# Performance work log

Measured on AMD Instinct MI355X. Metric: run time of the kernel, lower is better.

## Reference

```python
import jax, jax.numpy as jnp
import numpy as np

INPUT_SIZE = 64 * 64 * 10  # 40960
H1, H2, H3 = 256, 32, 32
BATCH = 2048


def _linear_init(key, out_f, in_f):
    # torch nn.Linear default init: U(-1/sqrt(in_f), 1/sqrt(in_f))
    kw, kb = jax.random.split(key)
    bound = 1.0 / np.sqrt(in_f)
    W = jax.random.uniform(kw, (out_f, in_f), jnp.float32, -bound, bound)
    b = jax.random.uniform(kb, (out_f,), jnp.float32, -bound, bound)
    return W, b


def setup_inputs() -> dict:
    key = jax.random.key(0)
    ks = jax.random.split(key, 7)
    input_player = jax.random.uniform(ks[0], (BATCH, INPUT_SIZE), jnp.float32)
    input_opponent = jax.random.uniform(ks[1], (BATCH, INPUT_SIZE), jnp.float32)
    W1p, b1p = _linear_init(ks[2], H1, INPUT_SIZE)
    W1o, b1o = _linear_init(ks[3], H1, INPUT_SIZE)
    W2, b2 = _linear_init(ks[4], H2, 2 * H1)
    W3, b3 = _linear_init(ks[5], H3, H2)
    Wo, bo = _linear_init(ks[6], 1, H3)
    return {
        "input_player": input_player, "input_opponent": input_opponent,
        "W1p": W1p, "b1p": b1p, "W1o": W1o, "b1o": b1o,
        "W2": W2, "b2": b2, "W3": W3, "b3": b3, "Wo": Wo, "bo": bo,
    }


def _crelu(x):
    # ReLU followed by clamp(0, 1) == clipped ReLU
    return jnp.clip(x, 0.0, 1.0)


def reference(input_player, input_opponent, W1p, b1p, W1o, b1o, W2, b2, W3, b3, Wo, bo):
    # Feature transformer (sparse-in-practice 40960 -> 256 per perspective)
    acc_p = _crelu(input_player @ W1p.T + b1p)    # [B, 256]
    acc_o = _crelu(input_opponent @ W1o.T + b1o)  # [B, 256]
    combined = jnp.concatenate([acc_p, acc_o], axis=-1)  # [B, 512]
    h = _crelu(combined @ W2.T + b2)  # [B, 32]
    h = _crelu(h @ W3.T + b3)         # [B, 32]
    out = _crelu(h @ Wo.T + bo)       # [B, 1]
    return out
```

## Files before the change

kernel.cpp:

```cpp
#include <hip/hip_runtime.h>

#define K_DIM 40960
#define NFEAT 256
#define BATCH 2048

typedef _Float16 f16;
typedef _Float16 f16x8 __attribute__((ext_vector_type(8)));
typedef _Float16 f16x4 __attribute__((ext_vector_type(4)));
typedef _Float16 f16x2 __attribute__((ext_vector_type(2)));
typedef float f32x4 __attribute__((ext_vector_type(4)));

__global__ __launch_bounds__(256) void convert_w(
    const float* __restrict__ w1p, const float* __restrict__ w1o,
    f16* __restrict__ w16p, f16* __restrict__ w16o) {
  const long N4 = (long)NFEAT * K_DIM / 4;
  long stride = (long)gridDim.x * blockDim.x;
  for (long i = (long)blockIdx.x * blockDim.x + threadIdx.x; i < 2 * N4; i += stride) {
    const float4* src;
    f16* dst;
    long idx;
    if (i < N4) { src = (const float4*)w1p; dst = w16p; idx = i; }
    else        { src = (const float4*)w1o; dst = w16o; idx = i - N4; }
    float4 v = src[idx];
    f16x4 h;
    h[0] = (f16)v.x; h[1] = (f16)v.y; h[2] = (f16)v.z; h[3] = (f16)v.w;
    *(f16x4*)(dst + idx * 4) = h;
  }
}

__global__ __launch_bounds__(512, 4) void ft_gemm(
    const float* __restrict__ Ap, const float* __restrict__ Ao,
    const f16* __restrict__ W16p, const f16* __restrict__ W16o,
    int S, f16* __restrict__ partials) {
  __shared__ f16 Ash[64 * 64];
  __shared__ f16 Wsh[256 * 64];

  const int b = blockIdx.x;
  const int G = 2 * S;
  const int g = b % G;
  const int mt = b / G;
  const int persp = g & 1;
  const int s = g >> 1;
  const int mbase = mt * 64;

  const float* A = persp ? Ao : Ap;
  const f16* W16 = persp ? W16o : W16p;

  const int tid = threadIdx.x;
  const int lane = tid & 63;
  const int wv = tid >> 6;
  const int mrow = lane & 15;
  const int kq = lane >> 4;

  f32x4 acc[4][2];
#pragma unroll
  for (int rt = 0; rt < 4; ++rt)
#pragma unroll
    for (int ct = 0; ct < 2; ++ct)
      acc[rt][ct] = (f32x4){0.f, 0.f, 0.f, 0.f};

  const int krange = K_DIM / S;
  const int kstart = s * krange;
  const int kend = kstart + krange;

  int a_row[2], a_cb[2];
#pragma unroll
  for (int i = 0; i < 2; ++i) { int f = i * 512 + tid; a_row[i] = f >> 4; a_cb[i] = f & 15; }
  int w_rl[4], w_kbs[4], w_kbg[4];
#pragma unroll
  for (int i = 0; i < 4; ++i) {
    int f = i * 512 + tid; w_rl[i] = f >> 3; w_kbs[i] = f & 7; w_kbg[i] = w_kbs[i] ^ (w_rl[i] & 7);
  }

  float4 pa[2];
  f16x8 pw[4];
#pragma unroll
  for (int i = 0; i < 2; ++i)
    pa[i] = *(const float4*)(A + (size_t)(mbase + a_row[i]) * K_DIM + kstart + a_cb[i] * 4);
#pragma unroll
  for (int i = 0; i < 4; ++i)
    pw[i] = *(const f16x8*)(W16 + (size_t)w_rl[i] * K_DIM + kstart + w_kbg[i] * 8);

  for (int k0 = kstart; k0 < kend; k0 += 64) {
#pragma unroll
    for (int i = 0; i < 2; ++i) {
      int row = a_row[i], cb = a_cb[i];
      int slot = (cb >> 1) ^ (row & 7);
      f16x4 h;
      h[0] = (f16)pa[i].x; h[1] = (f16)pa[i].y; h[2] = (f16)pa[i].z; h[3] = (f16)pa[i].w;
      *(f16x4*)&Ash[row * 64 + slot * 8 + (cb & 1) * 4] = h;
    }
#pragma unroll
    for (int i = 0; i < 4; ++i)
      *(f16x8*)&Wsh[w_rl[i] * 64 + w_kbs[i] * 8] = pw[i];
    __syncthreads();

    const int kn = (k0 + 64 < kend) ? (k0 + 64) : kstart;
#pragma unroll
    for (int i = 0; i < 2; ++i)
      pa[i] = *(const float4*)(A + (size_t)(mbase + a_row[i]) * K_DIM + kn + a_cb[i] * 4);
#pragma unroll
    for (int i = 0; i < 4; ++i)
      pw[i] = *(const f16x8*)(W16 + (size_t)w_rl[i] * K_DIM + kn + w_kbg[i] * 8);

#pragma unroll
    for (int ks = 0; ks < 2; ++ks) {
      const int kb = ks * 4 + kq;
      f16x8 af[4], bf[2];
#pragma unroll
      for (int rt = 0; rt < 4; ++rt) {
        int row = rt * 16 + mrow;
        af[rt] = *(const f16x8*)&Ash[row * 64 + (kb ^ (row & 7)) * 8];
      }
#pragma unroll
      for (int ct = 0; ct < 2; ++ct) {
        int rown = (wv * 2 + ct) * 16 + mrow;
        bf[ct] = *(const f16x8*)&Wsh[rown * 64 + (kb ^ (rown & 7)) * 8];
      }
#pragma unroll
      for (int rt = 0; rt < 4; ++rt)
#pragma unroll
        for (int ct = 0; ct < 2; ++ct)
          acc[rt][ct] = __builtin_amdgcn_mfma_f32_16x16x32_f16(af[rt], bf[ct], acc[rt][ct], 0, 0, 0);
    }
    __syncthreads();
  }

  f16* pp = partials + (size_t)g * ((size_t)BATCH * NFEAT);
#pragma unroll
  for (int rt = 0; rt < 4; ++rt)
#pragma unroll
    for (int ct = 0; ct < 2; ++ct) {
      int col = (wv * 2 + ct) * 16 + mrow;
#pragma unroll
      for (int i = 0; i < 4; ++i) {
        int row = mbase + rt * 16 + kq * 4 + i;
        pp[(size_t)row * NFEAT + col] = (f16)acc[rt][ct][i];
      }
    }
}

__global__ __launch_bounds__(256) void reduce_bias(
    const f16* __restrict__ partials, const float* __restrict__ b1p,
    const float* __restrict__ b1o, int S, float* __restrict__ combined) {
  int idx = blockIdx.x * 256 + threadIdx.x;
  int r = idx >> 8;
  int c2 = idx & 255;
  int persp = c2 >> 7;
  int n = (c2 & 127) * 2;
  const float* bias = persp ? b1o : b1p;
  float s0 = bias[n], s1 = bias[n + 1];
#pragma unroll 4
  for (int s = 0; s < S; ++s) {
    f16x2 v = *(const f16x2*)(partials + ((size_t)(s * 2 + persp)) * BATCH * NFEAT +
                              (size_t)r * NFEAT + n);
    s0 += (float)v[0]; s1 += (float)v[1];
  }
  s0 = fminf(fmaxf(s0, 0.f), 1.f);
  s1 = fminf(fmaxf(s1, 0.f), 1.f);
  float2 o; o.x = s0; o.y = s1;
  *(float2*)(combined + (size_t)r * 512 + persp * 256 + n) = o;
}

__global__ __launch_bounds__(256) void mlp(
    const float* __restrict__ combined, const float* __restrict__ W2,
    const float* __restrict__ b2, const float* __restrict__ W3,
    const float* __restrict__ b3, const float* __restrict__ Wo,
    const float* __restrict__ bo, float* __restrict__ out) {
  __shared__ f16 W2T[512 * 33];
  __shared__ float H1s[8][33];
  __shared__ float H2s[8][33];
  int tid = threadIdx.x;
#pragma unroll
  for (int i = 0; i < 64; ++i) {
    int idx = i * 256 + tid;
    int j = idx >> 9;
    int k = idx & 511;
    W2T[k * 33 + j] = (f16)W2[idx];
  }
  __syncthreads();

  int lr = tid >> 5;
  int j = tid & 31;
  int r = blockIdx.x * 8 + lr;

  const float* crow = combined + (size_t)r * 512;
  float acc = b2[j];
#pragma unroll 8
  for (int k = 0; k < 512; ++k) acc += crow[k] * (float)W2T[k * 33 + j];
  H1s[lr][j] = fminf(fmaxf(acc, 0.f), 1.f);
  __syncthreads();

  acc = b3[j];
  const float* w3r = W3 + j * 32;
#pragma unroll
  for (int k = 0; k < 32; ++k) acc += H1s[lr][k] * w3r[k];
  H2s[lr][j] = fminf(fmaxf(acc, 0.f), 1.f);
  __syncthreads();

  if (j == 0) {
    float o = bo[0];
#pragma unroll
    for (int k = 0; k < 32; ++k) o += H2s[lr][k] * Wo[k];
    out[r] = fminf(fmaxf(o, 0.f), 1.f);
  }
}

extern "C" void kernel_launch(void* const* d_in, const int* in_sizes, int n_in,
                              void* d_out, int out_size, void* d_ws, size_t ws_size,
                              hipStream_t stream) {
  const float* Ap  = (const float*)d_in[0];
  const float* Ao  = (const float*)d_in[1];
  const float* W1p = (const float*)d_in[2];
  const float* b1p = (const float*)d_in[3];
  const float* W1o = (const float*)d_in[4];
  const float* b1o = (const float*)d_in[5];
  const float* W2  = (const float*)d_in[6];
  const float* b2  = (const float*)d_in[7];
  const float* W3  = (const float*)d_in[8];
  const float* b3  = (const float*)d_in[9];
  const float* Wo  = (const float*)d_in[10];
  const float* bo  = (const float*)d_in[11];
  float* out = (float*)d_out;

  const size_t W16B = 2UL * NFEAT * K_DIM * 2;
  const size_t COMB = (size_t)BATCH * 512 * 4;
  auto need = [&](int s) {
    return W16B + (size_t)s * 2 * BATCH * NFEAT * 2 + COMB;
  };

  int S = 16;
  while (S > 1 && need(S) > ws_size) S >>= 1;

  char* ws = (char*)d_ws;
  f16* W16p = (f16*)ws;
  f16* W16o = W16p + (size_t)NFEAT * K_DIM;
  f16* partials = (f16*)(ws + W16B);
  float* combined = (float*)(ws + W16B + (size_t)S * 2 * BATCH * NFEAT * 2);

  convert_w<<<1024, 256, 0, stream>>>(W1p, W1o, W16p, W16o);

  int grid = (BATCH / 64) * S * 2;
  ft_gemm<<<grid, 512, 0, stream>>>(Ap, Ao, W16p, W16o, S, partials);

  reduce_bias<<<(BATCH * 256) / 256, 256, 0, stream>>>(partials, b1p, b1o, S, combined);

  mlp<<<BATCH / 8, 256, 0, stream>>>(combined, W2, b2, W3, b3, Wo, bo, out);
}
```

Before: 779.8 us.

## Keep W fragments in registers, double-buffer A tile, switch to 32x32 MFMA

The feature-transformer GEMM no longer stages the W tile through shared memory. Each wave now loads its 32-column W fragments straight from global memory into registers, with two register sets prefetched alternately. The A tile is double-buffered in LDS, so each iteration needs one barrier instead of two, and the MFMA shape changes from 16x16x32 to 32x32x16. The split-K factor drops from 16 to 8, which cuts partial-sum traffic and reduce work but leaves fewer blocks. This trades LDS traffic and barriers for higher register pressure and uncoalesced-per-row global W loads.

```diff
diff --git a/kernel.cpp b/kernel.cpp
--- a/kernel.cpp
+++ b/kernel.cpp
@@ -9,6 +9,7 @@
 typedef _Float16 f16x4 __attribute__((ext_vector_type(4)));
 typedef _Float16 f16x2 __attribute__((ext_vector_type(2)));
 typedef float f32x4 __attribute__((ext_vector_type(4)));
+typedef float f32x16 __attribute__((ext_vector_type(16)));
 
 __global__ __launch_bounds__(256) void convert_w(
     const float* __restrict__ w1p, const float* __restrict__ w1o,
@@ -32,8 +33,7 @@
     const float* __restrict__ Ap, const float* __restrict__ Ao,
     const f16* __restrict__ W16p, const f16* __restrict__ W16o,
     int S, f16* __restrict__ partials) {
-  __shared__ f16 Ash[64 * 64];
-  __shared__ f16 Wsh[256 * 64];
+  __shared__ f16 Ash[2][64 * 64];
 
   const int b = blockIdx.x;
   const int G = 2 * S;
@@ -49,94 +49,115 @@
   const int tid = threadIdx.x;
   const int lane = tid & 63;
   const int wv = tid >> 6;
-  const int mrow = lane & 15;
-  const int kq = lane >> 4;
-
-  f32x4 acc[4][2];
-#pragma unroll
-  for (int rt = 0; rt < 4; ++rt)
-#pragma unroll
-    for (int ct = 0; ct < 2; ++ct)
-      acc[rt][ct] = (f32x4){0.f, 0.f, 0.f, 0.f};
+  const int l31 = lane & 31;
+  const int hi = lane >> 5;
 
   const int krange = K_DIM / S;
   const int kstart = s * krange;
-  const int kend = kstart + krange;
-
-  int a_row[2], a_cb[2];
-#pragma unroll
-  for (int i = 0; i < 2; ++i) { int f = i * 512 + tid; a_row[i] = f >> 4; a_cb[i] = f & 15; }
-  int w_rl[4], w_kbs[4], w_kbg[4];
-#pragma unroll
-  for (int i = 0; i < 4; ++i) {
-    int f = i * 512 + tid; w_rl[i] = f >> 3; w_kbs[i] = f & 7; w_kbg[i] = w_kbs[i] ^ (w_rl[i] & 7);
-  }
-
-  float4 pa[2];
-  f16x8 pw[4];
-#pragma unroll
-  for (int i = 0; i < 2; ++i)
-    pa[i] = *(const float4*)(A + (size_t)(mbase + a_row[i]) * K_DIM + kstart + a_cb[i] * 4);
-#pragma unroll
-  for (int i = 0; i < 4; ++i)
-    pw[i] = *(const f16x8*)(W16 + (size_t)w_rl[i] * K_DIM + kstart + w_kbg[i] * 8);
-
-  for (int k0 = kstart; k0 < kend; k0 += 64) {
-#pragma unroll
-    for (int i = 0; i < 2; ++i) {
-      int row = a_row[i], cb = a_cb[i];
-      int slot = (cb >> 1) ^ (row & 7);
-      f16x4 h;
-      h[0] = (f16)pa[i].x; h[1] = (f16)pa[i].y; h[2] = (f16)pa[i].z; h[3] = (f16)pa[i].w;
-      *(f16x4*)&Ash[row * 64 + slot * 8 + (cb & 1) * 4] = h;
+  const int nit = krange / 64;
+
+  const int f0 = tid, f1 = tid + 512;
+  const int ar0 = f0 >> 4, ac0 = f0 & 15;
+  const int ar1 = f1 >> 4, ac1 = f1 & 15;
+  const float* pA0 = A + (size_t)(mbase + ar0) * K_DIM + ac0 * 4;
+  const float* pA1 = A + (size_t)(mbase + ar1) * K_DIM + ac1 * 4;
+  const int st0 = ar0 * 64 + (((ac0 >> 1) ^ (ar0 & 7)) * 8) + (ac0 & 1) * 4;
+  const int st1 = ar1 * 64 + (((ac1 >> 1) ^ (ar1 & 7)) * 8) + (ac1 & 1) * 4;
+
+  const f16* Wb = W16 + (size_t)(wv * 32 + l31) * K_DIM + hi * 8;
+
+  const int r7 = l31 & 7;
+  const int rd0 = l31 * 64;
+  const int rd1 = (32 + l31) * 64;
+
+  f32x16 acc0, acc1;
+#pragma unroll
+  for (int i = 0; i < 16; ++i) { acc0[i] = 0.f; acc1[i] = 0.f; }
+
+  float4 pa0, pa1;
+  f16x8 pwA[4], pwB[4];
+
+#define LOADA(kk) do { \
+    pa0 = *(const float4*)(pA0 + (kk)); \
+    pa1 = *(const float4*)(pA1 + (kk)); \
+  } while (0)
+
+#define LOADW(dst, kk) do { \
+    dst[0] = *(const f16x8*)(Wb + (kk)); \
+    dst[1] = *(const f16x8*)(Wb + (kk) + 16); \
+    dst[2] = *(const f16x8*)(Wb + (kk) + 32); \
+    dst[3] = *(const f16x8*)(Wb + (kk) + 48); \
+  } while (0)
+
+#define STAGE(buf) do { \
+    f16x4 h0, h1; \
+    h0[0] = (f16)pa0.x; h0[1] = (f16)pa0.y; h0[2] = (f16)pa0.z; h0[3] = (f16)pa0.w; \
+    h1[0] = (f16)pa1.x; h1[1] = (f16)pa1.y; h1[2] = (f16)pa1.z; h1[3] = (f16)pa1.w; \
+    *(f16x4*)&Ash[buf][st0] = h0; \
+    *(f16x4*)&Ash[buf][st1] = h1; \
+  } while (0)
+
+#define BARRIER() do { \
+    asm volatile("s_waitcnt lgkmcnt(0)" ::: "memory"); \
+    __builtin_amdgcn_sched_barrier(0); \
+    __builtin_amdgcn_s_barrier(); \
+    __builtin_amdgcn_sched_barrier(0); \
+  } while (0)
+
+#define COMPUTE(buf, pw, knext) do { \
+    _Pragma("unroll") \
+    for (int ks = 0; ks < 4; ++ks) { \
+      const int so = ((ks * 2 + hi) ^ r7) * 8; \
+      f16x8 af0 = *(const f16x8*)&Ash[buf][rd0 + so]; \
+      f16x8 af1 = *(const f16x8*)&Ash[buf][rd1 + so]; \
+      acc0 = __builtin_amdgcn_mfma_f32_32x32x16_f16(af0, pw[ks], acc0, 0, 0, 0); \
+      acc1 = __builtin_amdgcn_mfma_f32_32x32x16_f16(af1, pw[ks], acc1, 0, 0, 0); \
+      pw[ks] = *(const f16x8*)(Wb + (knext) + ks * 16); \
+    } \
+  } while (0)
+
+  LOADA(kstart);
+  LOADW(pwA, kstart);
+  STAGE(0);
+  const int k1 = kstart + (nit > 1 ? 64 : 0);
+  LOADA(k1);
+  LOADW(pwB, k1);
+  BARRIER();
+
+  for (int t = 0; t < nit; t += 2) {
+    const int k0 = kstart + t * 64;
+    {
+      STAGE(1);
+      const int kn = (t + 2 < nit) ? (k0 + 128) : kstart;
+      LOADA(kn);
+      COMPUTE(0, pwA, kn);
+      BARRIER();
     }
-#pragma unroll
-    for (int i = 0; i < 4; ++i)
-      *(f16x8*)&Wsh[w_rl[i] * 64 + w_kbs[i] * 8] = pw[i];
-    __syncthreads();
-
-    const int kn = (k0 + 64 < kend) ? (k0 + 64) : kstart;
-#pragma unroll
-    for (int i = 0; i < 2; ++i)
-      pa[i] = *(const float4*)(A + (size_t)(mbase + a_row[i]) * K_DIM + kn + a_cb[i] * 4);
-#pragma unroll
-    for (int i = 0; i < 4; ++i)
-      pw[i] = *(const f16x8*)(W16 + (size_t)w_rl[i] * K_DIM + kn + w_kbg[i] * 8);
-
-#pragma unroll
-    for (int ks = 0; ks < 2; ++ks) {
-      const int kb = ks * 4 + kq;
-      f16x8 af[4], bf[2];
-#pragma unroll
-      for (int rt = 0; rt < 4; ++rt) {
-        int row = rt * 16 + mrow;
-        af[rt] = *(const f16x8*)&Ash[row * 64 + (kb ^ (row & 7)) * 8];
-      }
-#pragma unroll
-      for (int ct = 0; ct < 2; ++ct) {
-        int rown = (wv * 2 + ct) * 16 + mrow;
-        bf[ct] = *(const f16x8*)&Wsh[rown * 64 + (kb ^ (rown & 7)) * 8];
-      }
-#pragma unroll
-      for (int rt = 0; rt < 4; ++rt)
-#pragma unroll
-        for (int ct = 0; ct < 2; ++ct)
-          acc[rt][ct] = __builtin_amdgcn_mfma_f32_16x16x32_f16(af[rt], bf[ct], acc[rt][ct], 0, 0, 0);
+    {
+      STAGE(0);
+      const int kn = (t + 3 < nit) ? (k0 + 192) : kstart;
+      LOADA(kn);
+      COMPUTE(1, pwB, kn);
+      BARRIER();
     }
-    __syncthreads();
-  }
+  }
+
+#undef LOADA
+#undef LOADW
+#undef STAGE
+#undef BARRIER
+#undef COMPUTE
 
   f16* pp = partials + (size_t)g * ((size_t)BATCH * NFEAT);
-#pragma unroll
-  for (int rt = 0; rt < 4; ++rt)
-#pragma unroll
-    for (int ct = 0; ct < 2; ++ct) {
-      int col = (wv * 2 + ct) * 16 + mrow;
-#pragma unroll
-      for (int i = 0; i < 4; ++i) {
-        int row = mbase + rt * 16 + kq * 4 + i;
-        pp[(size_t)row * NFEAT + col] = (f16)acc[rt][ct][i];
-      }
+  const int col = wv * 32 + l31;
+  const int rbase = mbase + 4 * hi;
+#pragma unroll
+  for (int q = 0; q < 4; ++q)
+#pragma unroll
+    for (int i = 0; i < 4; ++i) {
+      const int row = rbase + q * 8 + i;
+      pp[(size_t)row * NFEAT + col] = (f16)acc0[q * 4 + i];
+      pp[(size_t)(row + 32) * NFEAT + col] = (f16)acc1[q * 4 + i];
     }
 }
 
@@ -229,7 +250,7 @@
     return W16B + (size_t)s * 2 * BATCH * NFEAT * 2 + COMB;
   };
 
-  int S = 16;
+  int S = 8;
   while (S > 1 && need(S) > ws_size) S >>= 1;
 
   char* ws = (char*)d_ws;
```

Result: slower. 850.9 us (+9.1%).
